# Performance work log

Hardware: AMD Instinct MI355X
Metric: run time of the kernel (lower is better)

Reference implementation:

```python
import jax, jax.numpy as jnp
import numpy as np

B, S, D, H, DH, TLEN, TD = 4, 1024, 1024, 16, 64, 256, 256
EPS = 1e-5


def layer_norm(x, g, b):
    m = jnp.mean(x, axis=-1, keepdims=True)
    v = jnp.mean((x - m) ** 2, axis=-1, keepdims=True)
    return (x - m) * jax.lax.rsqrt(v + EPS) * g + b


def rotate_half(x):
    x1, x2 = jnp.split(x, 2, axis=-1)
    return jnp.concatenate((-x2, x1), axis=-1)


def apply_rope(pos, t):
    # pos: [S, DH] -> [1, S, 1, DH]; t: [B, S, H, DH]
    p = pos[None, :, None, :]
    return t * jnp.cos(p) + rotate_half(t) * jnp.sin(p)


def mha(q_in, kv_in, in_w, in_b, out_w, out_b, n_heads):
    # standard nn.MultiheadAttention math (batch-first tensors here)
    d = q_in.shape[-1]
    dh = d // n_heads
    q = q_in @ in_w[:d].T + in_b[:d]
    k = kv_in @ in_w[d:2 * d].T + in_b[d:2 * d]
    v = kv_in @ in_w[2 * d:].T + in_b[2 * d:]
    q = q.reshape(q.shape[0], q.shape[1], n_heads, dh)
    k = k.reshape(k.shape[0], k.shape[1], n_heads, dh)
    v = v.reshape(v.shape[0], v.shape[1], n_heads, dh)
    scores = jnp.einsum('bihd,bjhd->bhij', q, k) / jnp.sqrt(jnp.asarray(dh, q.dtype))
    attn = jax.nn.softmax(scores, axis=-1)
    o = jnp.einsum('bhij,bjhd->bihd', attn, v)
    o = o.reshape(o.shape[0], o.shape[1], d)
    return o @ out_w.T + out_b


def setup_inputs():
    key = jax.random.key(0)
    ks = jax.random.split(key, 20)
    s = 0.02
    inp = {
        'x': jax.random.normal(ks[0], (B, S, D), jnp.float32),
        'text_emb': jax.random.normal(ks[1], (B, TLEN, D), jnp.float32),
        'time_emb': jax.random.normal(ks[2], (B, TD), jnp.float32),
    }
    # true RoPE position encoding, matching RotaryEmbedding.forward
    inv_freq = 1.0 / (10000 ** (jnp.arange(0, DH, 2, dtype=jnp.float32) / DH))
    freqs = jnp.arange(S, dtype=jnp.float32)[:, None] * inv_freq[None, :]
    inp['rotary_pos'] = jnp.concatenate((freqs, freqs), axis=-1)  # [S, DH]
    inp.update(
        ln1_g=jnp.ones((D,), jnp.float32), ln1_b=jnp.zeros((D,), jnp.float32),
        ln2_g=jnp.ones((D,), jnp.float32), ln2_b=jnp.zeros((D,), jnp.float32),
        ln3_g=jnp.ones((D,), jnp.float32), ln3_b=jnp.zeros((D,), jnp.float32),
        attn_in_w=jax.random.normal(ks[3], (3 * D, D), jnp.float32) * s,
        attn_in_b=jnp.zeros((3 * D,), jnp.float32),
        ca_in_w=jax.random.normal(ks[4], (3 * D, D), jnp.float32) * s,
        ca_in_b=jnp.zeros((3 * D,), jnp.float32),
        ca_out_w=jax.random.normal(ks[5], (D, D), jnp.float32) * s,
        ca_out_b=jnp.zeros((D,), jnp.float32),
        fc1_w=jax.random.normal(ks[6], (4 * D, D), jnp.float32) * s,
        fc1_b=jnp.zeros((4 * D,), jnp.float32),
        gate_w=jax.random.normal(ks[7], (4 * D, D), jnp.float32) * s,
        gate_b=jnp.zeros((4 * D,), jnp.float32),
        fc2_w=jax.random.normal(ks[8], (D, 4 * D), jnp.float32) * s,
        fc2_b=jnp.zeros((D,), jnp.float32),
    )
    return inp


def reference(x, text_emb, time_emb, rotary_pos,
              ln1_g, ln1_b, ln2_g, ln2_b, ln3_g, ln3_b,
              attn_in_w, attn_in_b,
              ca_in_w, ca_in_b, ca_out_w, ca_out_b,
              fc1_w, fc1_b, gate_w, gate_b, fc2_w, fc2_b):
    b, n, d = x.shape
    # --- self-attention with manual RoPE (NOTE: original skips out_proj) ---
    residual = x
    xn = layer_norm(x, ln1_g, ln1_b)
    q = xn @ attn_in_w[:d].T + attn_in_b[:d]
    k = xn @ attn_in_w[d:2 * d].T + attn_in_b[d:2 * d]
    v = xn @ attn_in_w[2 * d:].T + attn_in_b[2 * d:]
    q = q.reshape(b, n, H, DH)
    k = k.reshape(b, n, H, DH)
    v = v.reshape(b, n, H, DH)
    q = apply_rope(rotary_pos, q)
    k = apply_rope(rotary_pos, k)
    scores = jnp.einsum('bihd,bjhd->bhij', q, k) / jnp.sqrt(jnp.asarray(DH, x.dtype))
    attn = jax.nn.softmax(scores, axis=-1)
    attn_out = jnp.einsum('bhij,bjhd->bihd', attn, v).reshape(b, n, d)
    x = attn_out + residual
    # --- cross-attention (full MHA, dropout inactive at eval) ---
    residual = x
    xn = layer_norm(x, ln2_g, ln2_b)
    x = mha(xn, text_emb, ca_in_w, ca_in_b, ca_out_w, ca_out_b, H) + residual
    # --- gated MLP ---
    residual = x
    xn = layer_norm(x, ln3_g, ln3_b)
    h = jax.nn.gelu(xn @ fc1_w.T + fc1_b, approximate=False)
    g = jax.nn.sigmoid(xn @ gate_w.T + gate_b)
    return (h * g) @ fc2_w.T + fc2_b + residual
```

## Files before the change

### kernel.cpp

```cpp
#include <hip/hip_runtime.h>
#include <hip/hip_bf16.h>

#define SEQ 1024
#define DIM 1024
#define NH 16

typedef __bf16 bf16_t;
typedef __bf16 bf16x8 __attribute__((ext_vector_type(8)));
typedef __bf16 bf16x4 __attribute__((ext_vector_type(4)));
typedef float f32x4 __attribute__((ext_vector_type(4)));

__device__ __forceinline__ f32x4 mfma16(bf16x8 a, bf16x8 b, f32x4 c) {
    return __builtin_amdgcn_mfma_f32_16x16x32_bf16(a, b, c, 0, 0, 0);
}

__device__ __forceinline__ void gload16(const bf16_t* g, bf16_t* l) {
    __builtin_amdgcn_global_load_lds(
        (const __attribute__((address_space(1))) void*)g,
        (__attribute__((address_space(3))) void*)l, 16, 0, 0);
}

enum { EPI_BF16 = 0, EPI_F32_RESID = 1 };

__global__ __launch_bounds__(256) void cvt_all(
    const float* __restrict__ s0, bf16_t* __restrict__ d0,
    const float* __restrict__ s1, bf16_t* __restrict__ d1,
    const float* __restrict__ s2, bf16_t* __restrict__ d2,
    const float* __restrict__ s3, bf16_t* __restrict__ d3,
    const float* __restrict__ s4, bf16_t* __restrict__ d4,
    const float* __restrict__ s5, bf16_t* __restrict__ d5,
    const float* __restrict__ s6, bf16_t* __restrict__ d6) {
    const int b = blockIdx.x;
    const float* s;
    bf16_t* d;
    int off;
    if (b < 3072) { s = s0; d = d0; off = b; }
    else if (b < 6144) { s = s1; d = d1; off = b - 3072; }
    else if (b < 7168) { s = s2; d = d2; off = b - 6144; }
    else if (b < 11264) { s = s3; d = d3; off = b - 7168; }
    else if (b < 15360) { s = s4; d = d4; off = b - 11264; }
    else if (b < 19456) { s = s5; d = d5; off = b - 15360; }
    else { s = s6; d = d6; off = b - 19456; }
    const int i = off * 256 + threadIdx.x;
    const float4 v = ((const float4*)s)[i];
    bf16x4 o = {(bf16_t)v.x, (bf16_t)v.y, (bf16_t)v.z, (bf16_t)v.w};
    ((bf16x4*)d)[i] = o;
}

__global__ __launch_bounds__(256) void ln_kernel(const float* __restrict__ in,
                                                 const float* __restrict__ g,
                                                 const float* __restrict__ bsh,
                                                 bf16_t* __restrict__ out) {
    __shared__ float red[4], red2[4];
    const int row = blockIdx.x, tid = threadIdx.x;
    const float4 v = ((const float4*)(in + (size_t)row * DIM))[tid];
    float s = v.x + v.y + v.z + v.w;
#pragma unroll
    for (int o = 32; o; o >>= 1) s += __shfl_down(s, o, 64);
    if ((tid & 63) == 0) red[tid >> 6] = s;
    __syncthreads();
    const float mean = (red[0] + red[1] + red[2] + red[3]) * (1.0f / DIM);
    const float dx = v.x - mean, dy = v.y - mean, dz = v.z - mean, dw = v.w - mean;
    float s2 = dx * dx + dy * dy + dz * dz + dw * dw;
#pragma unroll
    for (int o = 32; o; o >>= 1) s2 += __shfl_xor(s2, o, 64);
    if ((tid & 63) == 0) red2[tid >> 6] = s2;
    __syncthreads();
    const float var = (red2[0] + red2[1] + red2[2] + red2[3]) * (1.0f / DIM);
    const float rs = rsqrtf(var + 1e-5f);
    const float4 gv = ((const float4*)g)[tid];
    const float4 bv = ((const float4*)bsh)[tid];
    bf16x4 o4 = {(bf16_t)(dx * rs * gv.x + bv.x), (bf16_t)(dy * rs * gv.y + bv.y),
                 (bf16_t)(dz * rs * gv.z + bv.z), (bf16_t)(dw * rs * gv.w + bv.w)};
    ((bf16x4*)(out + (size_t)row * DIM))[tid] = o4;
}

__global__ __launch_bounds__(256) void rope_kernel(bf16_t* __restrict__ qkv,
                                                   const float* __restrict__ rp) {
    const int t = blockIdx.x * 256 + threadIdx.x;
    const int row = t >> 9;
    const int rem = t & 511;
    const int h = rem >> 5, d = rem & 31;
    const int s = row & (SEQ - 1);
    const float p0 = rp[s * 64 + d];
    const float p1 = rp[s * 64 + d + 32];
    float s0, c0, s1, c1;
    sincosf(p0, &s0, &c0);
    sincosf(p1, &s1, &c1);
    const size_t base = (size_t)row * 3072 + h * 64 + d;
#pragma unroll
    for (int off = 0; off <= 1024; off += 1024) {
        const float a = (float)qkv[base + off];
        const float b = (float)qkv[base + off + 32];
        qkv[base + off] = (bf16_t)(a * c0 - b * s0);
        qkv[base + off + 32] = (bf16_t)(b * c1 + a * s1);
    }
}

__device__ __forceinline__ float epi_apply_gelu(float v) {
    return 0.5f * v * (1.0f + erff(v * 0.70710678118f));
}

__global__ __launch_bounds__(256) void vtrans_kernel(
    const bf16_t* __restrict__ src, int ld, int voff, int skv,
    bf16_t* __restrict__ vt) {
    __shared__ bf16_t T[64 * 72];
    const int qt = blockIdx.x, h = blockIdx.y, b = blockIdx.z;
    const int tid = threadIdx.x;
    const int s0 = qt * 64;
#pragma unroll
    for (int t = 0; t < 2; ++t) {
        const int idx = t * 256 + tid;
        const int r = idx >> 3, c8 = (idx & 7) * 8;
        bf16x8 v = *(const bf16x8*)(src + (size_t)(b * skv + s0 + r) * ld +
                                    voff + h * 64 + c8);
        *(bf16x8*)&T[r * 72 + c8] = v;
    }
    __syncthreads();
    const size_t base = ((size_t)(b * NH + h) * 64) * skv;
#pragma unroll
    for (int t = 0; t < 2; ++t) {
        const int idx = t * 256 + tid;
        const int d = idx >> 3, s8 = (idx & 7) * 8;
        bf16x8 w;
#pragma unroll
        for (int i = 0; i < 8; ++i) w[i] = T[(s8 + i) * 72 + d];
        *(bf16x8*)(vt + base + (size_t)d * skv + s0 + s8) = w;
    }
}

#define ALD 72
template <bool OUTBF>
__global__ __launch_bounds__(512) void attn3_kernel(
    const bf16_t* __restrict__ qp, int ldq, int qoff,
    const bf16_t* __restrict__ kp, int ldk, int koff,
    const bf16_t* __restrict__ vtp, int skv,
    const float* __restrict__ resid, void* __restrict__ outp, float scale) {
    __shared__ bf16_t Ks[4096];
    __shared__ bf16_t Vs[4096];
    __shared__ bf16_t Ps[8 * 16 * ALD];
    const int nwg = gridDim.x;
    const int t = (blockIdx.x & 7) * (nwg >> 3) + (blockIdx.x >> 3);
    const int qt = t & 7;
    const int bh = t >> 3;
    const int b = bh >> 4, h = bh & 15;
    const int tid = threadIdx.x;
    const int wave = tid >> 6, lane = tid & 63;
    const int lr = lane & 15, hi = lane >> 4;

    const size_t qrow = (size_t)(b * SEQ + qt * 128 + wave * 16 + lr);
    const bf16_t* qb = qp + qrow * ldq + qoff + h * 64;
    const bf16x8 qf0 = *(const bf16x8*)(qb + hi * 8);
    const bf16x8 qf1 = *(const bf16x8*)(qb + 32 + hi * 8);

    const bf16_t* vbase = vtp + ((size_t)bh * 64) * skv;

    f32x4 oacc[4];
#pragma unroll
    for (int n = 0; n < 4; ++n) oacc[n] = (f32x4){0.f, 0.f, 0.f, 0.f};
    float mrun[4] = {-1e30f, -1e30f, -1e30f, -1e30f};
    float lrun[4] = {0.f, 0.f, 0.f, 0.f};

    bf16_t* pw = &Ps[wave * 16 * ALD];
    const int nkt = skv >> 6;
    for (int kt = 0; kt < nkt; ++kt) {
        {
            const int grow = (wave >> 1) * 16 + lr, gcol = (wave & 1) * 32 + hi * 8;
            gload16(kp + (size_t)(b * skv + kt * 64 + grow) * ldk + koff +
                        h * 64 + gcol,
                    &Ks[wave * 512]);
            gload16(vbase + (size_t)grow * skv + kt * 64 + gcol, &Vs[wave * 512]);
        }
        __syncthreads();

        f32x4 s[4];
#pragma unroll
        for (int n = 0; n < 4; ++n) {
            f32x4 z = (f32x4){0.f, 0.f, 0.f, 0.f};
            z = mfma16(qf0, *(const bf16x8*)&Ks[(n * 2 + 0) * 512 + lane * 8], z);
            z = mfma16(qf1, *(const bf16x8*)&Ks[(n * 2 + 1) * 512 + lane * 8], z);
            s[n] = z * scale;
        }
        float alpha[4];
#pragma unroll
        for (int j = 0; j < 4; ++j) {
            float mt = fmaxf(fmaxf(s[0][j], s[1][j]), fmaxf(s[2][j], s[3][j]));
#pragma unroll
            for (int o = 8; o >= 1; o >>= 1) mt = fmaxf(mt, __shfl_xor(mt, o, 64));
            const float mnew = fmaxf(mrun[j], mt);
            alpha[j] = __expf(mrun[j] - mnew);
            float rsum = 0.f;
#pragma unroll
            for (int n = 0; n < 4; ++n) {
                const float p = __expf(s[n][j] - mnew);
                s[n][j] = p;
                rsum += p;
            }
#pragma unroll
            for (int o = 8; o >= 1; o >>= 1) rsum += __shfl_xor(rsum, o, 64);
            lrun[j] = lrun[j] * alpha[j] + rsum;
            mrun[j] = mnew;
        }
#pragma unroll
        for (int j = 0; j < 4; ++j) {
            const int pr = hi * 4 + j;
#pragma unroll
            for (int n = 0; n < 4; ++n) pw[pr * ALD + n * 16 + lr] = (bf16_t)s[n][j];
        }
#pragma unroll
        for (int n = 0; n < 4; ++n)
#pragma unroll
            for (int j = 0; j < 4; ++j) oacc[n][j] *= alpha[j];
#pragma unroll
        for (int ks = 0; ks < 2; ++ks) {
            const bf16x8 pa = *(const bf16x8*)&pw[lr * ALD + ks * 32 + hi * 8];
#pragma unroll
            for (int n = 0; n < 4; ++n) {
                const bf16x8 vf =
                    *(const bf16x8*)&Vs[(n * 2 + ks) * 512 + lane * 8];
                oacc[n] = mfma16(pa, vf, oacc[n]);
            }
        }
        __syncthreads();
    }

    const size_t orow0 = (size_t)(b * SEQ + qt * 128 + wave * 16);
#pragma unroll
    for (int n = 0; n < 4; ++n) {
#pragma unroll
        for (int j = 0; j < 4; ++j) {
            const int r = hi * 4 + j;
            const size_t idx = (orow0 + r) * DIM + h * 64 + n * 16 + lr;
            float val = oacc[n][j] / lrun[j];
            if constexpr (OUTBF) {
                ((bf16_t*)outp)[idx] = (bf16_t)val;
            } else {
                ((float*)outp)[idx] = val + resid[idx];
            }
        }
    }
}

template <int EPI, int MODE>
__global__ __launch_bounds__(512, 4) void gemm8w(
    const bf16_t* __restrict__ A, int lda, const bf16_t* __restrict__ W, int ldw,
    const float* __restrict__ bias, const void* __restrict__ aux,
    void* __restrict__ outv, int ldo, int K, int nM) {
    __shared__ bf16_t As[2][8192];
    __shared__ bf16_t Bs[2][8192];
    const int tid = threadIdx.x;
    const int wave = tid >> 6, lane = tid & 63;
    const int wm = wave >> 2, wn = wave & 3;
    const int lr = lane & 15, hi = lane >> 4;

    const int x = blockIdx.x & 7, i = blockIdx.x >> 3;
    int mt, nt;
    if constexpr (MODE == 0) {
        const int mc = nM >> 3;
        mt = x * mc + (i % mc);
        nt = i / mc;
    } else {
        const int nc = (gridDim.x / nM) >> 3;
        nt = x * nc + (i % nc);
        mt = i / nc;
    }
    const int rowA0 = mt * 128, rowB0 = nt * 128;

    f32x4 acc[4][2];
#pragma unroll
    for (int m = 0; m < 4; ++m)
#pragma unroll
        for (int n = 0; n < 2; ++n) acc[m][n] = (f32x4){0.f, 0.f, 0.f, 0.f};

    auto stage = [&](int kt, int b) {
        const int k0 = kt * 64;
#pragma unroll
        for (int u = 0; u < 2; ++u) {
            const int c = wave * 2 + u;
            const int grow = wave * 16 + lr, gcol = k0 + u * 32 + hi * 8;
            gload16(A + (size_t)(rowA0 + grow) * lda + gcol, &As[b][c * 512]);
            gload16(W + (size_t)(rowB0 + grow) * ldw + gcol, &Bs[b][c * 512]);
        }
    };

    const int NT = K >> 6;
    stage(0, 0);
    stage(1, 1);
    asm volatile("s_waitcnt vmcnt(4)" ::: "memory");
    __builtin_amdgcn_s_barrier();

    for (int kt = 0; kt < NT; ++kt) {
        const int cur = kt & 1;
#pragma unroll
        for (int ks = 0; ks < 2; ++ks) {
            bf16x8 af[4], bfr[2];
#pragma unroll
            for (int mf = 0; mf < 4; ++mf)
                af[mf] = *(const bf16x8*)&As[cur][((wm * 4 + mf) * 2 + ks) * 512 +
                                                 hi * 128 + lr * 8];
#pragma unroll
            for (int nf = 0; nf < 2; ++nf)
                bfr[nf] = *(const bf16x8*)&Bs[cur][((wn * 2 + nf) * 2 + ks) * 512 +
                                                  hi * 128 + lr * 8];
#pragma unroll
            for (int mf = 0; mf < 4; ++mf)
#pragma unroll
                for (int nf = 0; nf < 2; ++nf)
                    acc[mf][nf] = mfma16(af[mf], bfr[nf], acc[mf][nf]);
        }
        if (kt + 1 < NT) {
            __builtin_amdgcn_sched_barrier(0);
            __builtin_amdgcn_s_barrier();
            if (kt + 2 < NT) {
                stage(kt + 2, cur);
                asm volatile("s_waitcnt vmcnt(4)" ::: "memory");
            } else {
                asm volatile("s_waitcnt vmcnt(0)" ::: "memory");
            }
            __builtin_amdgcn_s_barrier();
        }
    }

    float bn[2];
#pragma unroll
    for (int n = 0; n < 2; ++n) bn[n] = bias[rowB0 + wn * 32 + n * 16 + lr];
#pragma unroll
    for (int m = 0; m < 4; ++m) {
#pragma unroll
        for (int j = 0; j < 4; ++j) {
            const int row = rowA0 + wm * 64 + m * 16 + hi * 4 + j;
#pragma unroll
            for (int n = 0; n < 2; ++n) {
                const int col = rowB0 + wn * 32 + n * 16 + lr;
                float val = acc[m][n][j] + bn[n];
                const size_t oidx = (size_t)row * ldo + col;
                if constexpr (EPI == EPI_BF16) {
                    ((bf16_t*)outv)[oidx] = (bf16_t)val;
                } else {
                    ((float*)outv)[oidx] = val + ((const float*)aux)[oidx];
                }
            }
        }
    }
}

template <int EPI>
__global__ __launch_bounds__(256, 4) void gemm64(
    const bf16_t* __restrict__ A, int lda, const bf16_t* __restrict__ W, int ldw,
    const float* __restrict__ bias, const void* __restrict__ aux,
    void* __restrict__ outv, int ldo, int K, int nM) {
    __shared__ bf16_t As[2][4096];
    __shared__ bf16_t Bs[2][4096];
    const int tid = threadIdx.x;
    const int wave = tid >> 6, lane = tid & 63;
    const int wm = wave >> 1, wn = wave & 1;
    const int lr = lane & 15, hi = lane >> 4;

    const int x = blockIdx.x & 7, i = blockIdx.x >> 3;
    const int nc = (gridDim.x / nM) >> 3;
    const int nt = x * nc + (i % nc), mt = i / nc;
    const int rowA0 = mt * 64, rowB0 = nt * 64;

    f32x4 acc[2][2];
#pragma unroll
    for (int m = 0; m < 2; ++m)
#pragma unroll
        for (int n = 0; n < 2; ++n) acc[m][n] = (f32x4){0.f, 0.f, 0.f, 0.f};

    auto stage = [&](int kt, int b) {
        const int k0 = kt * 64;
#pragma unroll
        for (int u = 0; u < 2; ++u) {
            const int c = wave * 2 + u;
            const int grow = (c >> 1) * 16 + lr, gcol = k0 + (c & 1) * 32 + hi * 8;
            gload16(A + (size_t)(rowA0 + grow) * lda + gcol, &As[b][c * 512]);
            gload16(W + (size_t)(rowB0 + grow) * ldw + gcol, &Bs[b][c * 512]);
        }
    };

    const int NT = K >> 6;
    stage(0, 0);
    stage(1, 1);
    asm volatile("s_waitcnt vmcnt(4)" ::: "memory");
    __builtin_amdgcn_s_barrier();

    for (int kt = 0; kt < NT; ++kt) {
        const int cur = kt & 1;
#pragma unroll
        for (int ks = 0; ks < 2; ++ks) {
            bf16x8 af[2], bfr[2];
#pragma unroll
            for (int mf = 0; mf < 2; ++mf)
                af[mf] = *(const bf16x8*)&As[cur][((wm * 2 + mf) * 2 + ks) * 512 + lane * 8];
#pragma unroll
            for (int nf = 0; nf < 2; ++nf)
                bfr[nf] = *(const bf16x8*)&Bs[cur][((wn * 2 + nf) * 2 + ks) * 512 + lane * 8];
#pragma unroll
            for (int mf = 0; mf < 2; ++mf)
#pragma unroll
                for (int nf = 0; nf < 2; ++nf)
                    acc[mf][nf] = mfma16(af[mf], bfr[nf], acc[mf][nf]);
        }
        if (kt + 1 < NT) {
            __builtin_amdgcn_sched_barrier(0);
            __builtin_amdgcn_s_barrier();
            if (kt + 2 < NT) {
                stage(kt + 2, cur);
                asm volatile("s_waitcnt vmcnt(4)" ::: "memory");
            } else {
                asm volatile("s_waitcnt vmcnt(0)" ::: "memory");
            }
            __builtin_amdgcn_s_barrier();
        }
    }

    float bn[2];
#pragma unroll
    for (int n = 0; n < 2; ++n) bn[n] = bias[rowB0 + wn * 32 + n * 16 + lr];
#pragma unroll
    for (int m = 0; m < 2; ++m) {
#pragma unroll
        for (int j = 0; j < 4; ++j) {
            const int row = rowA0 + wm * 32 + m * 16 + hi * 4 + j;
#pragma unroll
            for (int n = 0; n < 2; ++n) {
                const int col = rowB0 + wn * 32 + n * 16 + lr;
                float val = acc[m][n][j] + bn[n];
                const size_t oidx = (size_t)row * ldo + col;
                if constexpr (EPI == EPI_BF16) {
                    ((bf16_t*)outv)[oidx] = (bf16_t)val;
                } else {
                    ((float*)outv)[oidx] = val + ((const float*)aux)[oidx];
                }
            }
        }
    }
}

__global__ __launch_bounds__(512, 4) void gemm_mlp(
    const bf16_t* __restrict__ A, int lda, const bf16_t* __restrict__ W1,
    const bf16_t* __restrict__ Wg, int ldw, const float* __restrict__ b1,
    const float* __restrict__ bg, bf16_t* __restrict__ outv, int ldo, int K,
    int nM) {
    __shared__ bf16_t As[2][8192];
    __shared__ bf16_t Bs[2][8192];
    const int tid = threadIdx.x;
    const int wave = tid >> 6, lane = tid & 63;
    const int wm = wave >> 2, wn = wave & 3;
    const int lr = lane & 15, hi = lane >> 4;

    const int x = blockIdx.x & 7, i = blockIdx.x >> 3;
    const int nc = (gridDim.x / nM) >> 3;
    const int nt = x * nc + (i % nc), mt = i / nc;
    const int rowA0 = mt * 128, colB0 = nt * 64;

    f32x4 acc[4][2];
#pragma unroll
    for (int m = 0; m < 4; ++m)
#pragma unroll
        for (int n = 0; n < 2; ++n) acc[m][n] = (f32x4){0.f, 0.f, 0.f, 0.f};

    const bf16_t* Wsrc = (wave & 1) ? Wg : W1;
    const int wrow = colB0 + (wave >> 1) * 16 + lr;
    auto stage = [&](int kt, int b) {
        const int k0 = kt * 64;
#pragma unroll
        for (int u = 0; u < 2; ++u) {
            const int c = wave * 2 + u;
            const int gcol = k0 + u * 32 + hi * 8;
            gload16(A + (size_t)(rowA0 + wave * 16 + lr) * lda + gcol,
                    &As[b][c * 512]);
            gload16(Wsrc + (size_t)wrow * ldw + gcol, &Bs[b][c * 512]);
        }
    };

    const int NT = K >> 6;
    stage(0, 0);
    stage(1, 1);
    asm volatile("s_waitcnt vmcnt(4)" ::: "memory");
    __builtin_amdgcn_s_barrier();

    for (int kt = 0; kt < NT; ++kt) {
        const int cur = kt & 1;
#pragma unroll
        for (int ks = 0; ks < 2; ++ks) {
            bf16x8 af[4], bh, bg_;
#pragma unroll
            for (int mf = 0; mf < 4; ++mf)
                af[mf] = *(const bf16x8*)&As[cur][((wm * 4 + mf) * 2 + ks) * 512 +
                                                 hi * 128 + lr * 8];
            bh = *(const bf16x8*)&Bs[cur][((2 * wn) * 2 + ks) * 512 + hi * 128 + lr * 8];
            bg_ = *(const bf16x8*)&Bs[cur][((2 * wn + 1) * 2 + ks) * 512 + hi * 128 + lr * 8];
#pragma unroll
            for (int mf = 0; mf < 4; ++mf) {
                acc[mf][0] = mfma16(af[mf], bh, acc[mf][0]);
                acc[mf][1] = mfma16(af[mf], bg_, acc[mf][1]);
            }
        }
        if (kt + 1 < NT) {
            __builtin_amdgcn_sched_barrier(0);
            __builtin_amdgcn_s_barrier();
            if (kt + 2 < NT) {
                stage(kt + 2, cur);
                asm volatile("s_waitcnt vmcnt(4)" ::: "memory");
            } else {
                asm volatile("s_waitcnt vmcnt(0)" ::: "memory");
            }
            __builtin_amdgcn_s_barrier();
        }
    }

    const int col = colB0 + wn * 16 + lr;
    const float bb1 = b1[col], bbg = bg[col];
#pragma unroll
    for (int m = 0; m < 4; ++m) {
#pragma unroll
        for (int j = 0; j < 4; ++j) {
            const int row = rowA0 + wm * 64 + m * 16 + hi * 4 + j;
            const float h = acc[m][0][j] + bb1;
            const float g = acc[m][1][j] + bbg;
            const float sg = 1.0f / (1.0f + __expf(-g));
            outv[(size_t)row * ldo + col] = (bf16_t)(epi_apply_gelu(h) * sg);
        }
    }
}

extern "C" void kernel_launch(void* const* d_in, const int* in_sizes, int n_in,
                              void* d_out, int out_size, void* d_ws, size_t ws_size,
                              hipStream_t stream) {
    const float* x = (const float*)d_in[0];
    const float* text_emb = (const float*)d_in[1];
    const float* rotary = (const float*)d_in[3];
    const float* ln1_g = (const float*)d_in[4];
    const float* ln1_b = (const float*)d_in[5];
    const float* ln2_g = (const float*)d_in[6];
    const float* ln2_b = (const float*)d_in[7];
    const float* ln3_g = (const float*)d_in[8];
    const float* ln3_b = (const float*)d_in[9];
    const float* attn_in_w = (const float*)d_in[10];
    const float* attn_in_b = (const float*)d_in[11];
    const float* ca_in_w = (const float*)d_in[12];
    const float* ca_in_b = (const float*)d_in[13];
    const float* ca_out_w = (const float*)d_in[14];
    const float* ca_out_b = (const float*)d_in[15];
    const float* fc1_w = (const float*)d_in[16];
    const float* fc1_b = (const float*)d_in[17];
    const float* gate_w = (const float*)d_in[18];
    const float* gate_b = (const float*)d_in[19];
    const float* fc2_w = (const float*)d_in[20];
    const float* fc2_b = (const float*)d_in[21];

    char* ws = (char*)d_ws;
    bf16_t* attn_w_bf = (bf16_t*)(ws);
    bf16_t* ca_in_bf = (bf16_t*)(ws + 6291456);
    bf16_t* ca_out_bf = (bf16_t*)(ws + 12582912);
    bf16_t* fc1_bf = (bf16_t*)(ws + 14680064);
    bf16_t* gate_bf = (bf16_t*)(ws + 23068672);
    bf16_t* fc2_bf = (bf16_t*)(ws + 31457280);
    bf16_t* text_bf = (bf16_t*)(ws + 39845888);
    bf16_t* xn = (bf16_t*)(ws + 41943040);
    float* xA = (float*)(ws + 50331648);
    char* S = ws + 67108864;
    bf16_t* qkv = (bf16_t*)S;
    bf16_t* vtSelf = (bf16_t*)(S + 25165824);
    bf16_t* cq = (bf16_t*)S;
    bf16_t* ckv = (bf16_t*)(S + 8388608);
    bf16_t* ca_attn = (bf16_t*)(S + 12582912);
    bf16_t* vtCross = (bf16_t*)(S + 20971520);
    bf16_t* hbuf = (bf16_t*)S;
    float* out = (float*)d_out;

    cvt_all<<<20480, 256, 0, stream>>>(attn_in_w, attn_w_bf, ca_in_w, ca_in_bf,
                                       ca_out_w, ca_out_bf, fc1_w, fc1_bf,
                                       gate_w, gate_bf, fc2_w, fc2_bf,
                                       text_emb, text_bf);

    ln_kernel<<<4096, 256, 0, stream>>>(x, ln1_g, ln1_b, xn);
    gemm8w<EPI_BF16, 0><<<768, 512, 0, stream>>>(
        xn, 1024, attn_w_bf, 1024, attn_in_b, nullptr, qkv, 3072, 1024, 32);
    rope_kernel<<<8192, 256, 0, stream>>>(qkv, rotary);
    vtrans_kernel<<<dim3(16, 16, 4), 256, 0, stream>>>(qkv, 3072, 2048, 1024, vtSelf);
    attn3_kernel<false><<<512, 512, 0, stream>>>(
        qkv, 3072, 0, qkv, 3072, 1024, vtSelf, 1024, x, xA, 0.125f);

    ln_kernel<<<4096, 256, 0, stream>>>(xA, ln2_g, ln2_b, xn);
    gemm8w<EPI_BF16, 0><<<256, 512, 0, stream>>>(
        xn, 1024, ca_in_bf, 1024, ca_in_b, nullptr, cq, 1024, 1024, 32);
    gemm8w<EPI_BF16, 1><<<128, 512, 0, stream>>>(
        text_bf, 1024, ca_in_bf + (size_t)1024 * 1024, 1024, ca_in_b + 1024, nullptr,
        ckv, 2048, 1024, 8);
    vtrans_kernel<<<dim3(4, 16, 4), 256, 0, stream>>>(ckv, 2048, 1024, 256, vtCross);
    attn3_kernel<true><<<512, 512, 0, stream>>>(
        cq, 1024, 0, ckv, 2048, 0, vtCross, 256, nullptr, ca_attn, 0.125f);
    gemm8w<EPI_F32_RESID, 0><<<256, 512, 0, stream>>>(
        ca_attn, 1024, ca_out_bf, 1024, ca_out_b, xA, xA, 1024, 1024, 32);

    ln_kernel<<<4096, 256, 0, stream>>>(xA, ln3_g, ln3_b, xn);
    gemm_mlp<<<2048, 512, 0, stream>>>(
        xn, 1024, fc1_bf, gate_bf, 1024, fc1_b, gate_b, hbuf, 4096, 1024, 32);
    gemm64<EPI_F32_RESID><<<1024, 256, 0, stream>>>(
        hbuf, 4096, fc2_bf, 4096, fc2_b, xA, out, 1024, 4096, 64);
}
```

Measured before the change: 530.4 us.

## Use 128x128-tile split-K GEMM with separate reduce kernel for fc2

Replaces the 64x64-tile fc2 GEMM with an 8-wave kernel that computes 128x128 output tiles. K is split in two halves, and each half writes fp32 partial sums. A new elementwise kernel then adds the two partials, the bias and the residual. The aim is more operand reuse per block while keeping enough blocks in flight for the long K=4096 reduction. The cost is an extra 16MB fp32 partial buffer, an additional launch, and the memory traffic of the reduce pass. The partial buffer reuses the fc1/gate weight workspace, which is safe only because those weights are no longer needed at that point.

```diff
diff --git a/kernel.cpp b/kernel.cpp
--- a/kernel.cpp
+++ b/kernel.cpp
@@ -344,41 +344,44 @@
     }
 }
 
-template <int EPI>
-__global__ __launch_bounds__(256, 4) void gemm64(
+__global__ __launch_bounds__(512, 4) void gemm8w_sk(
     const bf16_t* __restrict__ A, int lda, const bf16_t* __restrict__ W, int ldw,
-    const float* __restrict__ bias, const void* __restrict__ aux,
-    void* __restrict__ outv, int ldo, int K, int nM) {
-    __shared__ bf16_t As[2][4096];
-    __shared__ bf16_t Bs[2][4096];
+    float* __restrict__ p0, float* __restrict__ p1, int ldo, int Khalf, int nM) {
+    __shared__ bf16_t As[2][8192];
+    __shared__ bf16_t Bs[2][8192];
     const int tid = threadIdx.x;
     const int wave = tid >> 6, lane = tid & 63;
-    const int wm = wave >> 1, wn = wave & 1;
+    const int wm = wave >> 2, wn = wave & 3;
     const int lr = lane & 15, hi = lane >> 4;
 
-    const int x = blockIdx.x & 7, i = blockIdx.x >> 3;
-    const int nc = (gridDim.x / nM) >> 3;
-    const int nt = x * nc + (i % nc), mt = i / nc;
-    const int rowA0 = mt * 64, rowB0 = nt * 64;
-
-    f32x4 acc[2][2];
-#pragma unroll
-    for (int m = 0; m < 2; ++m)
+    const int sk = blockIdx.x >> 8;
+    const int bi = blockIdx.x & 255;
+    const int x = bi & 7, i = bi >> 3;
+    const int mc = nM >> 3;
+    const int mt = x * mc + (i % mc);
+    const int nt = i / mc;
+    const int rowA0 = mt * 128, rowB0 = nt * 128;
+    const int kbase = sk * Khalf;
+    float* outp = sk ? p1 : p0;
+
+    f32x4 acc[4][2];
+#pragma unroll
+    for (int m = 0; m < 4; ++m)
 #pragma unroll
         for (int n = 0; n < 2; ++n) acc[m][n] = (f32x4){0.f, 0.f, 0.f, 0.f};
 
     auto stage = [&](int kt, int b) {
-        const int k0 = kt * 64;
+        const int k0 = kbase + kt * 64;
 #pragma unroll
         for (int u = 0; u < 2; ++u) {
             const int c = wave * 2 + u;
-            const int grow = (c >> 1) * 16 + lr, gcol = k0 + (c & 1) * 32 + hi * 8;
+            const int grow = wave * 16 + lr, gcol = k0 + u * 32 + hi * 8;
             gload16(A + (size_t)(rowA0 + grow) * lda + gcol, &As[b][c * 512]);
             gload16(W + (size_t)(rowB0 + grow) * ldw + gcol, &Bs[b][c * 512]);
         }
     };
 
-    const int NT = K >> 6;
+    const int NT = Khalf >> 6;
     stage(0, 0);
     stage(1, 1);
     asm volatile("s_waitcnt vmcnt(4)" ::: "memory");
@@ -388,15 +391,17 @@
         const int cur = kt & 1;
 #pragma unroll
         for (int ks = 0; ks < 2; ++ks) {
-            bf16x8 af[2], bfr[2];
-#pragma unroll
-            for (int mf = 0; mf < 2; ++mf)
-                af[mf] = *(const bf16x8*)&As[cur][((wm * 2 + mf) * 2 + ks) * 512 + lane * 8];
+            bf16x8 af[4], bfr[2];
+#pragma unroll
+            for (int mf = 0; mf < 4; ++mf)
+                af[mf] = *(const bf16x8*)&As[cur][((wm * 4 + mf) * 2 + ks) * 512 +
+                                                 hi * 128 + lr * 8];
 #pragma unroll
             for (int nf = 0; nf < 2; ++nf)
-                bfr[nf] = *(const bf16x8*)&Bs[cur][((wn * 2 + nf) * 2 + ks) * 512 + lane * 8];
-#pragma unroll
-            for (int mf = 0; mf < 2; ++mf)
+                bfr[nf] = *(const bf16x8*)&Bs[cur][((wn * 2 + nf) * 2 + ks) * 512 +
+                                                  hi * 128 + lr * 8];
+#pragma unroll
+            for (int mf = 0; mf < 4; ++mf)
 #pragma unroll
                 for (int nf = 0; nf < 2; ++nf)
                     acc[mf][nf] = mfma16(af[mf], bfr[nf], acc[mf][nf]);
@@ -414,27 +419,34 @@
         }
     }
 
-    float bn[2];
-#pragma unroll
-    for (int n = 0; n < 2; ++n) bn[n] = bias[rowB0 + wn * 32 + n * 16 + lr];
-#pragma unroll
-    for (int m = 0; m < 2; ++m) {
+#pragma unroll
+    for (int m = 0; m < 4; ++m) {
 #pragma unroll
         for (int j = 0; j < 4; ++j) {
-            const int row = rowA0 + wm * 32 + m * 16 + hi * 4 + j;
+            const int row = rowA0 + wm * 64 + m * 16 + hi * 4 + j;
 #pragma unroll
             for (int n = 0; n < 2; ++n) {
                 const int col = rowB0 + wn * 32 + n * 16 + lr;
-                float val = acc[m][n][j] + bn[n];
-                const size_t oidx = (size_t)row * ldo + col;
-                if constexpr (EPI == EPI_BF16) {
-                    ((bf16_t*)outv)[oidx] = (bf16_t)val;
-                } else {
-                    ((float*)outv)[oidx] = val + ((const float*)aux)[oidx];
-                }
-            }
-        }
-    }
+                outp[(size_t)row * ldo + col] = acc[m][n][j];
+            }
+        }
+    }
+}
+
+__global__ __launch_bounds__(256) void reduce_fc2(
+    float* __restrict__ outp, const float* __restrict__ p1,
+    const float* __restrict__ bias, const float* __restrict__ resid) {
+    const int i = blockIdx.x * 256 + threadIdx.x;
+    const float4 a = ((const float4*)outp)[i];
+    const float4 b = ((const float4*)p1)[i];
+    const float4 r = ((const float4*)resid)[i];
+    const float4 bv = ((const float4*)bias)[i & 255];
+    float4 o;
+    o.x = a.x + b.x + r.x + bv.x;
+    o.y = a.y + b.y + r.y + bv.y;
+    o.z = a.z + b.z + r.z + bv.z;
+    o.w = a.w + b.w + r.w + bv.w;
+    ((float4*)outp)[i] = o;
 }
 
 __global__ __launch_bounds__(512, 4) void gemm_mlp(
@@ -560,6 +572,7 @@
     bf16_t* text_bf = (bf16_t*)(ws + 39845888);
     bf16_t* xn = (bf16_t*)(ws + 41943040);
     float* xA = (float*)(ws + 50331648);
+    float* fc2_p1 = (float*)(ws + 14680064);
     char* S = ws + 67108864;
     bf16_t* qkv = (bf16_t*)S;
     bf16_t* vtSelf = (bf16_t*)(S + 25165824);
@@ -598,6 +611,7 @@
     ln_kernel<<<4096, 256, 0, stream>>>(xA, ln3_g, ln3_b, xn);
     gemm_mlp<<<2048, 512, 0, stream>>>(
         xn, 1024, fc1_bf, gate_bf, 1024, fc1_b, gate_b, hbuf, 4096, 1024, 32);
-    gemm64<EPI_F32_RESID><<<1024, 256, 0, stream>>>(
-        hbuf, 4096, fc2_bf, 4096, fc2_b, xA, out, 1024, 4096, 64);
-}
+    gemm8w_sk<<<512, 512, 0, stream>>>(
+        hbuf, 4096, fc2_bf, 4096, out, fc2_p1, 1024, 2048, 32);
+    reduce_fc2<<<4096, 256, 0, stream>>>(out, fc2_p1, fc2_b, xA);
+}
```

Measured after the change: 477.5 us (median of 2 runs). -10.0%, faster.
